# Kernel tuning notes

Measured on AMD Instinct MI355X. Metric: run time of the kernel, lower is better.

The kernel has to match this reference:

```python
import jax, jax.numpy as jnp
import numpy as np

D_K = 64

def setup_inputs() -> dict:
    key = jax.random.key(0)
    kq, kk, kv, kw = jax.random.split(key, 4)
    B, H, L, Dk, Dv = 16, 8, 1024, 64, 64
    Q = jax.random.normal(kq, (B, H, L, Dk), dtype=jnp.float32)
    K = jax.random.normal(kk, (B, H, L, Dk), dtype=jnp.float32)
    V = jax.random.normal(kv, (B, H, L, Dv), dtype=jnp.float32)
    W = jax.random.normal(kw, (H, L, 2 * Dk), dtype=jnp.float32)
    return {"Q": Q, "K": K, "V": V, "W": W}

def reference(Q, K, V, W):
    scale = 1.0 / jnp.sqrt(jnp.float32(D_K))
    # branch 1: standard scaled dot-product attention scores [B,H,Lq,Lk]
    scores = jnp.einsum('bhqd,bhkd->bhqk', Q, K) * scale
    attn = jax.nn.softmax(scores, axis=-1)
    # branch 2: learned-weight concat(Q,K) projection
    # W [H, Lq, 2Dk] @ cat(Q,K)^T [B,H,2Dk,Lk] -> [B,H,Lq,Lk]
    qk = jnp.concatenate([Q, K], axis=-1)  # [B,H,L,2Dk]
    scores_cat = jnp.einsum('hqc,bhkc->bhqk', W, qk) * scale
    attn_cat = jax.nn.softmax(scores_cat, axis=-1)
    attention = attn + attn_cat
    context = jnp.einsum('bhqk,bhkd->bhqd', attention, V)
    return context, attention
```

## Files before the change

### kernel.cpp

```cpp
#include <hip/hip_runtime.h>

#define L_SEQ 1024
#define DKV 64
#define NT 16

typedef float f32x4 __attribute__((ext_vector_type(4)));
typedef _Float16 f16x8 __attribute__((ext_vector_type(8)));
typedef _Float16 f16x4 __attribute__((ext_vector_type(4)));

#define QK_STRIDE 136
#define VT_STRIDE 76
#define ATT_STRIDE 80

__device__ __forceinline__ f32x4 mfma16(f16x8 a, f16x8 b, f32x4 c) {
    return __builtin_amdgcn_mfma_f32_16x16x32_f16(a, b, c, 0, 0, 0);
}

__device__ __forceinline__ float fast_exp2(float x) {
#if __has_builtin(__builtin_amdgcn_exp2f)
    return __builtin_amdgcn_exp2f(x);
#else
    return exp2f(x);
#endif
}

__global__ __launch_bounds__(512, 2)
void fused_dual_attn(const float* __restrict__ Qg, const float* __restrict__ Kg,
                     const float* __restrict__ Vg, const float* __restrict__ Wg,
                     float* __restrict__ out_ctx, float* __restrict__ out_att)
{
    __shared__ _Float16 qk_lds[2][64 * QK_STRIDE];
    __shared__ _Float16 vt_lds[2][64 * VT_STRIDE];
    __shared__ _Float16 att_lds[8][16 * ATT_STRIDE];

    const int tid  = (int)threadIdx.x;
    const int lane = tid & 63;
    const int w    = tid >> 6;
    const int a    = lane & 15;
    const int g    = lane >> 4;

    const int bid = (int)blockIdx.x;
    const int sw  = (bid & 7) * 128 + (bid >> 3);
    const int bh  = sw >> 3;
    const int q0  = (sw & 7) * 128;
    const int h   = bh & 7;

    const float SCALE_L2 = 0.125f * 1.44269504088896340736f;

    const float* Qh = Qg + (size_t)bh * (L_SEQ * DKV);
    const float* Kh = Kg + (size_t)bh * (L_SEQ * DKV);
    const float* Vh = Vg + (size_t)bh * (L_SEQ * DKV);
    const float* Wh = Wg + (size_t)h * (L_SEQ * 2 * DKV);

    f16x8 qa[2];
    f16x8 wa[4];
    {
        const int q = q0 + w * 16 + a;
        const float* qrow = Qh + q * DKV;
        const float* wrow = Wh + q * (2 * DKV);
#pragma unroll
        for (int kk = 0; kk < 2; ++kk) {
            const float* p = qrow + kk * 32 + g * 8;
            f32x4 lo = *(const f32x4*)p;
            f32x4 hi = *(const f32x4*)(p + 4);
            f16x8 v;
#pragma unroll
            for (int e = 0; e < 4; ++e) {
                v[e]     = (_Float16)(lo[e] * SCALE_L2);
                v[e + 4] = (_Float16)(hi[e] * SCALE_L2);
            }
            qa[kk] = v;
        }
#pragma unroll
        for (int kk = 0; kk < 4; ++kk) {
            const float* p = wrow + kk * 32 + g * 8;
            f32x4 lo = *(const f32x4*)p;
            f32x4 hi = *(const f32x4*)(p + 4);
            f16x8 v;
#pragma unroll
            for (int e = 0; e < 4; ++e) {
                v[e]     = (_Float16)(lo[e] * SCALE_L2);
                v[e + 4] = (_Float16)(hi[e] * SCALE_L2);
            }
            wa[kk] = v;
        }
    }

    f32x4 qkreg[4];
    auto qk_load = [&](int t) {
#pragma unroll
        for (int i = 0; i < 4; ++i) {
            int u   = tid + i * 512;
            int row = u >> 5;
            int c   = (u & 31) * 4;
            const float* src = (c < 64) ? (Qh + (t * 64 + row) * DKV + c)
                                        : (Kh + (t * 64 + row) * DKV + (c - 64));
            qkreg[i] = *(const f32x4*)src;
        }
    };
    auto qk_store = [&](int b) {
#pragma unroll
        for (int i = 0; i < 4; ++i) {
            int u   = tid + i * 512;
            int row = u >> 5;
            int c   = (u & 31) * 4;
            f16x4 y;
#pragma unroll
            for (int e = 0; e < 4; ++e) y[e] = (_Float16)qkreg[i][e];
            *(f16x4*)&qk_lds[b][row * QK_STRIDE + c] = y;
        }
    };

    f32x4 vreg[4];
    auto vt_load = [&](int t) {
        const int kq = tid >> 4;
        const int dc = tid & 15;
        const float* base = Vh + (t * 64 + 4 * kq) * DKV + 4 * dc;
#pragma unroll
        for (int j = 0; j < 4; ++j) vreg[j] = *(const f32x4*)(base + j * DKV);
    };
    auto vt_store = [&](int b) {
        const int kq = tid >> 4;
        const int dc = tid & 15;
#pragma unroll
        for (int i = 0; i < 4; ++i) {
            f16x4 y = { (_Float16)vreg[0][i], (_Float16)vreg[1][i],
                        (_Float16)vreg[2][i], (_Float16)vreg[3][i] };
            *(f16x4*)&vt_lds[b][(4 * dc + i) * VT_STRIDE + 4 * kq] = y;
        }
    };

    auto compute_scores = [&](int b, f32x4 (&s1)[4], f32x4 (&s2)[4]) {
        f16x8 kb[4][2], qb[4][2];
#pragma unroll
        for (int fc = 0; fc < 4; ++fc) {
            const _Float16* rowp = &qk_lds[b][(fc * 16 + a) * QK_STRIDE];
#pragma unroll
            for (int kk = 0; kk < 2; ++kk) {
                qb[fc][kk] = *(const f16x8*)(rowp + kk * 32 + g * 8);
                kb[fc][kk] = *(const f16x8*)(rowp + 64 + kk * 32 + g * 8);
            }
        }
        const f32x4 cinit = { -13.0f, -13.0f, -13.0f, -13.0f };
        __builtin_amdgcn_s_setprio(1);
#pragma unroll
        for (int fc = 0; fc < 4; ++fc) {
            f32x4 acc = cinit;
            acc = mfma16(qa[0], kb[fc][0], acc);
            acc = mfma16(qa[1], kb[fc][1], acc);
            s1[fc] = acc;
            f32x4 acc2 = cinit;
            acc2 = mfma16(wa[0], qb[fc][0], acc2);
            acc2 = mfma16(wa[1], qb[fc][1], acc2);
            acc2 = mfma16(wa[2], kb[fc][0], acc2);
            acc2 = mfma16(wa[3], kb[fc][1], acc2);
            s2[fc] = acc2;
        }
        __builtin_amdgcn_s_setprio(0);
    };

    float lsum1[4] = {0.f, 0.f, 0.f, 0.f};
    float lsum2[4] = {0.f, 0.f, 0.f, 0.f};
    qk_load(0);
    qk_store(0);
    __syncthreads();
    for (int t = 0; t < NT; ++t) {
        if (t < NT - 1) qk_load(t + 1);
        f32x4 s1[4], s2[4];
        compute_scores(t & 1, s1, s2);
#pragma unroll
        for (int fc = 0; fc < 4; ++fc)
#pragma unroll
            for (int r = 0; r < 4; ++r) {
                lsum1[r] += fast_exp2(s1[fc][r]);
                lsum2[r] += fast_exp2(s2[fc][r]);
            }
        if (t < NT - 1) qk_store((t + 1) & 1);
        __syncthreads();
    }

    float rinv1[4], rinv2[4];
#pragma unroll
    for (int r = 0; r < 4; ++r) {
#pragma unroll
        for (int m = 1; m <= 8; m <<= 1) {
            lsum1[r] += __shfl_xor(lsum1[r], m, 64);
            lsum2[r] += __shfl_xor(lsum2[r], m, 64);
        }
        rinv1[r] = 1.0f / lsum1[r];
        rinv2[r] = 1.0f / lsum2[r];
    }

    f32x4 ctx[4] = {{0.f,0.f,0.f,0.f},{0.f,0.f,0.f,0.f},
                    {0.f,0.f,0.f,0.f},{0.f,0.f,0.f,0.f}};
    float* att_base = out_att + (size_t)bh * L_SEQ * L_SEQ;
    _Float16* patt = &att_lds[w][0];

    qk_load(0);
    if (tid < 256) vt_load(0);
    qk_store(0);
    if (tid < 256) vt_store(0);
    __syncthreads();
    for (int t = 0; t < NT; ++t) {
        if (t < NT - 1) { qk_load(t + 1); if (tid < 256) vt_load(t + 1); }
        f32x4 s1[4], s2[4];
        compute_scores(t & 1, s1, s2);
#pragma unroll
        for (int fc = 0; fc < 4; ++fc)
#pragma unroll
            for (int r = 0; r < 4; ++r) {
                const int ql = 4 * g + r;
                float av = fast_exp2(s1[fc][r]) * rinv1[r]
                         + fast_exp2(s2[fc][r]) * rinv2[r];
                att_base[(size_t)(q0 + w * 16 + ql) * L_SEQ + t * 64 + fc * 16 + a] = av;
                patt[ql * ATT_STRIDE + fc * 16 + a] = (_Float16)av;
            }
        __builtin_amdgcn_s_setprio(1);
#pragma unroll
        for (int kk = 0; kk < 2; ++kk) {
            f16x8 pa = *(const f16x8*)&patt[a * ATT_STRIDE + kk * 32 + g * 8];
#pragma unroll
            for (int fc2 = 0; fc2 < 4; ++fc2) {
                f16x8 vb = *(const f16x8*)&vt_lds[t & 1][(fc2 * 16 + a) * VT_STRIDE + kk * 32 + g * 8];
                ctx[fc2] = mfma16(pa, vb, ctx[fc2]);
            }
        }
        __builtin_amdgcn_s_setprio(0);
        if (t < NT - 1) { qk_store((t + 1) & 1); if (tid < 256) vt_store((t + 1) & 1); }
        __syncthreads();
    }

    float* ctx_base = out_ctx + (size_t)bh * L_SEQ * DKV;
#pragma unroll
    for (int fc2 = 0; fc2 < 4; ++fc2)
#pragma unroll
        for (int r = 0; r < 4; ++r) {
            const int q = q0 + w * 16 + 4 * g + r;
            const int d = fc2 * 16 + a;
            ctx_base[(size_t)q * DKV + d] = ctx[fc2][r];
        }
}

extern "C" void kernel_launch(void* const* d_in, const int* in_sizes, int n_in,
                              void* d_out, int out_size, void* d_ws, size_t ws_size,
                              hipStream_t stream) {
    const float* Q = (const float*)d_in[0];
    const float* K = (const float*)d_in[1];
    const float* V = (const float*)d_in[2];
    const float* W = (const float*)d_in[3];
    float* out_ctx = (float*)d_out;
    float* out_att = out_ctx + (size_t)16 * 8 * 1024 * 64;
    fused_dual_attn<<<1024, 512, 0, stream>>>(Q, K, V, W, out_ctx, out_att);
}
```

Baseline: 775.5 us.

## Transpose score MFMA operands for row-contiguous vectorized attention stores

```diff
diff --git a/kernel.cpp b/kernel.cpp
--- a/kernel.cpp
+++ b/kernel.cpp
@@ -10,7 +10,7 @@
 
 #define QK_STRIDE 136
 #define VT_STRIDE 76
-#define ATT_STRIDE 80
+#define ATT_STRIDE 72
 
 __device__ __forceinline__ f32x4 mfma16(f16x8 a, f16x8 b, f32x4 c) {
     return __builtin_amdgcn_mfma_f32_16x16x32_f16(a, b, c, 0, 0, 0);
@@ -22,6 +22,13 @@
 #else
     return exp2f(x);
 #endif
+}
+
+__device__ __forceinline__ void barrier_lgkm() {
+    __builtin_amdgcn_sched_barrier(0);
+    asm volatile("s_waitcnt lgkmcnt(0)" ::: "memory");
+    __builtin_amdgcn_s_barrier();
+    __builtin_amdgcn_sched_barrier(0);
 }
 
 __global__ __launch_bounds__(512, 2)
@@ -146,21 +153,20 @@
 #pragma unroll
         for (int fc = 0; fc < 4; ++fc) {
             f32x4 acc = cinit;
-            acc = mfma16(qa[0], kb[fc][0], acc);
-            acc = mfma16(qa[1], kb[fc][1], acc);
+            acc = mfma16(kb[fc][0], qa[0], acc);
+            acc = mfma16(kb[fc][1], qa[1], acc);
             s1[fc] = acc;
             f32x4 acc2 = cinit;
-            acc2 = mfma16(wa[0], qb[fc][0], acc2);
-            acc2 = mfma16(wa[1], qb[fc][1], acc2);
-            acc2 = mfma16(wa[2], kb[fc][0], acc2);
-            acc2 = mfma16(wa[3], kb[fc][1], acc2);
+            acc2 = mfma16(qb[fc][0], wa[0], acc2);
+            acc2 = mfma16(qb[fc][1], wa[1], acc2);
+            acc2 = mfma16(kb[fc][0], wa[2], acc2);
+            acc2 = mfma16(kb[fc][1], wa[3], acc2);
             s2[fc] = acc2;
         }
         __builtin_amdgcn_s_setprio(0);
     };
 
-    float lsum1[4] = {0.f, 0.f, 0.f, 0.f};
-    float lsum2[4] = {0.f, 0.f, 0.f, 0.f};
+    float lsum1 = 0.f, lsum2 = 0.f;
     qk_load(0);
     qk_store(0);
     __syncthreads();
@@ -172,28 +178,24 @@
         for (int fc = 0; fc < 4; ++fc)
 #pragma unroll
             for (int r = 0; r < 4; ++r) {
-                lsum1[r] += fast_exp2(s1[fc][r]);
-                lsum2[r] += fast_exp2(s2[fc][r]);
+                lsum1 += fast_exp2(s1[fc][r]);
+                lsum2 += fast_exp2(s2[fc][r]);
             }
         if (t < NT - 1) qk_store((t + 1) & 1);
-        __syncthreads();
+        barrier_lgkm();
     }
 
-    float rinv1[4], rinv2[4];
-#pragma unroll
-    for (int r = 0; r < 4; ++r) {
-#pragma unroll
-        for (int m = 1; m <= 8; m <<= 1) {
-            lsum1[r] += __shfl_xor(lsum1[r], m, 64);
-            lsum2[r] += __shfl_xor(lsum2[r], m, 64);
-        }
-        rinv1[r] = 1.0f / lsum1[r];
-        rinv2[r] = 1.0f / lsum2[r];
-    }
+    lsum1 += __shfl_xor(lsum1, 16, 64);
+    lsum1 += __shfl_xor(lsum1, 32, 64);
+    lsum2 += __shfl_xor(lsum2, 16, 64);
+    lsum2 += __shfl_xor(lsum2, 32, 64);
+    const float rinv1 = 1.0f / lsum1;
+    const float rinv2 = 1.0f / lsum2;
 
     f32x4 ctx[4] = {{0.f,0.f,0.f,0.f},{0.f,0.f,0.f,0.f},
                     {0.f,0.f,0.f,0.f},{0.f,0.f,0.f,0.f}};
-    float* att_base = out_att + (size_t)bh * L_SEQ * L_SEQ;
+    float* att_row = out_att + (size_t)bh * L_SEQ * L_SEQ
+                             + (size_t)(q0 + w * 16 + a) * L_SEQ;
     _Float16* patt = &att_lds[w][0];
 
     qk_load(0);
@@ -206,15 +208,16 @@
         f32x4 s1[4], s2[4];
         compute_scores(t & 1, s1, s2);
 #pragma unroll
-        for (int fc = 0; fc < 4; ++fc)
-#pragma unroll
-            for (int r = 0; r < 4; ++r) {
-                const int ql = 4 * g + r;
-                float av = fast_exp2(s1[fc][r]) * rinv1[r]
-                         + fast_exp2(s2[fc][r]) * rinv2[r];
-                att_base[(size_t)(q0 + w * 16 + ql) * L_SEQ + t * 64 + fc * 16 + a] = av;
-                patt[ql * ATT_STRIDE + fc * 16 + a] = (_Float16)av;
-            }
+        for (int fc = 0; fc < 4; ++fc) {
+            f32x4 avv;
+#pragma unroll
+            for (int r = 0; r < 4; ++r)
+                avv[r] = fast_exp2(s1[fc][r]) * rinv1 + fast_exp2(s2[fc][r]) * rinv2;
+            *(f32x4*)&att_row[t * 64 + fc * 16 + g * 4] = avv;
+            f16x4 ph = { (_Float16)avv[0], (_Float16)avv[1],
+                         (_Float16)avv[2], (_Float16)avv[3] };
+            *(f16x4*)&patt[a * ATT_STRIDE + fc * 16 + g * 4] = ph;
+        }
         __builtin_amdgcn_s_setprio(1);
 #pragma unroll
         for (int kk = 0; kk < 2; ++kk) {
@@ -227,7 +230,7 @@
         }
         __builtin_amdgcn_s_setprio(0);
         if (t < NT - 1) { qk_store((t + 1) & 1); if (tid < 256) vt_store((t + 1) & 1); }
-        __syncthreads();
+        barrier_lgkm();
     }
 
     float* ctx_base = out_ctx + (size_t)bh * L_SEQ * DKV;
```

Result: faster. 759.7 us (-2.0%).
